# Performance work log

Measured on AMD Instinct MI355X. Metric: run time of the kernel, lower is better.

Reference implementation:

```python
import jax, jax.numpy as jnp
import numpy as np

B, N, E, H = 8, 512, 256, 8
HD = E // H
FF = 4 * E
TOPK = max(1, int(N * 0.2))
FW_MAX_DIST = 10      # default of get_shortest_path_matrix
EMB_MAX_IDX = 6       # spd encoder: max_dist(5) + 1
LN_EPS = 1e-5


def _layernorm(x, g, b):
    m = jnp.mean(x, axis=-1, keepdims=True)
    v = jnp.var(x, axis=-1, keepdims=True)
    return (x - m) / jnp.sqrt(v + LN_EPS) * g + b


def setup_inputs() -> dict:
    key = jax.random.key(0)
    ks = jax.random.split(key, 12)
    s = 0.02
    return {
        "x": jax.random.normal(ks[0], (B, N, E), jnp.float32),
        "adj": jax.random.uniform(ks[1], (B, N, N), jnp.float32),
        "emb_spd": (jax.random.normal(ks[2], (EMB_MAX_IDX + 1, H), jnp.float32) * s),
        "w_qkv": jax.random.normal(ks[3], (3 * E, E), jnp.float32) * s,
        "b_qkv": jnp.zeros((3 * E,), jnp.float32),
        "w_out": jax.random.normal(ks[4], (E, E), jnp.float32) * s,
        "b_out": jnp.zeros((E,), jnp.float32),
        "w_ff1": jax.random.normal(ks[5], (FF, E), jnp.float32) * s,
        "b_ff1": jnp.zeros((FF,), jnp.float32),
        "w_ff2": jax.random.normal(ks[6], (E, FF), jnp.float32) * s,
        "b_ff2": jnp.zeros((E,), jnp.float32),
        "g1": jnp.ones((E,), jnp.float32),
        "beta1": jnp.zeros((E,), jnp.float32),
        "g2": jnp.ones((E,), jnp.float32),
        "beta2": jnp.zeros((E,), jnp.float32),
        "w_pool": jax.random.normal(ks[7], (1, E), jnp.float32) * s,
        "b_pool": jnp.zeros((1,), jnp.float32),
    }


def _combined_mask(adj, emb_spd):
    # top-k per row -> binary adjacency via scatter
    _, idx = jax.lax.top_k(adj, TOPK)                       # [B,N,k]
    bi = jnp.arange(B)[:, None, None]
    ri = jnp.arange(N)[None, :, None]
    binary = jnp.zeros_like(adj).at[bi, ri, idx].set(1.0)   # [B,N,N]

    # Floyd-Warshall shortest paths
    dist = jnp.where(binary == 1.0, 1.0, jnp.inf)
    ids = jnp.arange(N)
    dist = dist.at[:, ids, ids].set(0.0)

    def body(k, d):
        return jnp.minimum(d, d[:, :, k][:, :, None] + d[:, k, :][:, None, :])

    dist = jax.lax.fori_loop(0, N, body, dist)
    dist_i = jnp.where(dist > FW_MAX_DIST, -1.0, dist).astype(jnp.int32)

    # spatial bias embedding: indices = clamp(dist+1, 0, max_dist+1)
    sp_idx = jnp.clip(dist_i + 1, 0, EMB_MAX_IDX)           # [B,N,N]
    bias = jnp.transpose(emb_spd[sp_idx], (0, 3, 1, 2))     # [B,H,N,N]

    base = jnp.where(binary == 0.0, -jnp.inf, 0.0)[:, None] # [B,1,N,N]
    return base + bias                                      # [B,H,N,N]


def reference(x, adj, emb_spd, w_qkv, b_qkv, w_out, b_out,
              w_ff1, b_ff1, w_ff2, b_ff2, g1, beta1, g2, beta2,
              w_pool, b_pool):
    mask = _combined_mask(adj, emb_spd)                     # [B,H,N,N]

    # multi-head self-attention (PyTorch MHA, post-norm encoder layer, eval)
    qkv = x @ w_qkv.T + b_qkv                               # [B,N,3E]
    q, k, v = jnp.split(qkv, 3, axis=-1)
    q = q.reshape(B, N, H, HD).transpose(0, 2, 1, 3)
    k = k.reshape(B, N, H, HD).transpose(0, 2, 1, 3)
    v = v.reshape(B, N, H, HD).transpose(0, 2, 1, 3)
    scores = jnp.einsum("bhqd,bhkd->bhqk", q, k) / np.sqrt(HD) + mask
    attn = jax.nn.softmax(scores, axis=-1)
    ctx = jnp.einsum("bhqk,bhkd->bhqd", attn, v)
    ctx = ctx.transpose(0, 2, 1, 3).reshape(B, N, E)
    attn_out = ctx @ w_out.T + b_out

    x1 = _layernorm(x + attn_out, g1, beta1)
    ff = jax.nn.relu(x1 @ w_ff1.T + b_ff1) @ w_ff2.T + b_ff2
    x2 = _layernorm(x1 + ff, g2, beta2)

    # attention pooling over nodes
    w = jax.nn.softmax(jnp.tanh(x2 @ w_pool.T + b_pool), axis=1)  # [B,N,1]
    return jnp.sum(x2 * w, axis=1)                          # [B,E]
```

## Files before the change

### kernel.cpp

```cpp
#include <hip/hip_runtime.h>
#include <math.h>


#define B_ 8
#define N_ 512
#define E_ 256
#define H_ 8
#define HD_ 32
#define TOPK_ 102

typedef __attribute__((ext_vector_type(8))) short bf16x8;
typedef __attribute__((ext_vector_type(4))) float f32x4;

__device__ __forceinline__ unsigned short f2b(float f) {
  unsigned u = __builtin_bit_cast(unsigned, f);
  return (unsigned short)((u + 0x7FFFu + ((u >> 16) & 1u)) >> 16);
}

__global__ __launch_bounds__(256) void cvt_topk(
    const float* __restrict__ adj, unsigned int* __restrict__ bits,
    const float* __restrict__ x, const float* __restrict__ wqkv,
    const float* __restrict__ wout, const float* __restrict__ wff1,
    const float* __restrict__ wff2, unsigned short* __restrict__ xb,
    unsigned short* __restrict__ wqkvb, unsigned short* __restrict__ woutb,
    unsigned short* __restrict__ wff1b, unsigned short* __restrict__ wff2b) {
  __shared__ unsigned int hist[1024];
  __shared__ float cval[64];
  __shared__ int cidx[64];
  __shared__ int s_cnt, s_bb, s_need;
  __shared__ unsigned int rowbits[16];
  __shared__ int wsum[4];
  const int t = threadIdx.x;

  if (blockIdx.x >= 4096) {
    int i = ((blockIdx.x - 4096) * 256 + t) * 4;
    const float* src;
    unsigned short* dst;
    int off;
    if (i < 1048576)      { src = x;    dst = xb;    off = i; }
    else if (i < 1245184) { src = wqkv; dst = wqkvb; off = i - 1048576; }
    else if (i < 1310720) { src = wout; dst = woutb; off = i - 1245184; }
    else if (i < 1572864) { src = wff1; dst = wff1b; off = i - 1310720; }
    else                  { src = wff2; dst = wff2b; off = i - 1572864; }
    float4 v = *(const float4*)(src + off);
    ushort4 o;
    o.x = f2b(v.x); o.y = f2b(v.y); o.z = f2b(v.z); o.w = f2b(v.w);
    *(ushort4*)(dst + off) = o;
    return;
  }
  const int row = blockIdx.x;
  const float* a = adj + (size_t)row * N_;
  const int lane = t & 63;
  const int wave = t >> 6;

  hist[t] = 0u; hist[t + 256] = 0u; hist[t + 512] = 0u; hist[t + 768] = 0u;
  if (t == 0) s_cnt = 0;
  float v0 = a[t];
  float v1 = a[t + 256];
  __syncthreads();
  const int b0 = min(1023, max(0, (int)(v0 * 1024.0f)));
  const int b1 = min(1023, max(0, (int)(v1 * 1024.0f)));
  atomicAdd(&hist[b0], 1u);
  atomicAdd(&hist[b1], 1u);
  __syncthreads();
  const int base = 1020 - 4 * t;
  const int h0 = (int)hist[base], h1 = (int)hist[base + 1];
  const int h2 = (int)hist[base + 2], h3 = (int)hist[base + 3];
  const int g = h0 + h1 + h2 + h3;
  int sc = g;
  #pragma unroll
  for (int off = 1; off < 64; off <<= 1) {
    int y = __shfl_up(sc, off);
    sc += (lane >= off) ? y : 0;
  }
  if (lane == 63) wsum[wave] = sc;
  __syncthreads();
  int wo = 0;
  for (int w = 0; w < wave; w++) wo += wsum[w];
  const int incl = sc + wo;
  const int excl = incl - g;
  if (excl < TOPK_ && incl >= TOPK_) {
    int cum = excl;
    int bb = base;
    const int hh[4] = {h3, h2, h1, h0};
    const int bs[4] = {base + 3, base + 2, base + 1, base};
    #pragma unroll
    for (int u = 0; u < 4; u++) {
      if (cum + hh[u] >= TOPK_) { bb = bs[u]; break; }
      cum += hh[u];
    }
    s_bb = bb;
    s_need = TOPK_ - cum;
  }
  __syncthreads();
  const int bb = s_bb;
  const int need = s_need;
  const bool sel0 = (b0 > bb);
  const bool sel1 = (b1 > bb);
  if (b0 == bb) { int p = atomicAdd(&s_cnt, 1); if (p < 64) { cval[p] = v0; cidx[p] = t; } }
  if (b1 == bb) { int p = atomicAdd(&s_cnt, 1); if (p < 64) { cval[p] = v1; cidx[p] = t + 256; } }
  unsigned long long m0 = __ballot(sel0);
  unsigned long long m1 = __ballot(sel1);
  if (lane == 0) {
    rowbits[2 * wave + 0] = (unsigned int)m0;
    rowbits[2 * wave + 1] = (unsigned int)(m0 >> 32);
    rowbits[8 + 2 * wave + 0] = (unsigned int)m1;
    rowbits[8 + 2 * wave + 1] = (unsigned int)(m1 >> 32);
  }
  __syncthreads();
  const int cnt = min(s_cnt, 64);
  for (int c = t; c < cnt; c += 256) {
    const float v = cval[c];
    const int idx = cidx[c];
    int r = 0;
    for (int j = 0; j < cnt; j++) {
      const float vj = cval[j];
      const int ij = cidx[j];
      if (vj > v || (vj == v && ij < idx)) r++;
    }
    if (r < need) atomicOr(&rowbits[idx >> 5], 1u << (idx & 31));
  }
  __syncthreads();
  if (t < 16) bits[(size_t)row * 16 + t] = rowbits[t];
}

__global__ __launch_bounds__(256) void gemm_mfma(
    const unsigned short* __restrict__ A, const unsigned short* __restrict__ W,
    const float* __restrict__ bias, const float* __restrict__ res,
    void* __restrict__ Cout, unsigned short* __restrict__ kG,
    unsigned short* __restrict__ vG, int M, int N, int K, int flags) {
  __shared__ __align__(16) unsigned short Af[8 * 64 * 8];
  __shared__ __align__(16) unsigned short Wf[8 * 64 * 8];
  const int tid = threadIdx.x;
  const int m0 = blockIdx.y * 64, n0 = blockIdx.x * 64;
  const int wave = tid >> 6, lane = tid & 63;
  const int wm = wave & 1, wn = wave >> 1;
  const int q = lane >> 4, l15 = lane & 15;
  const int r = tid >> 2, c0 = tid & 3;

  f32x4 acc[2][2];
  #pragma unroll
  for (int i = 0; i < 2; i++)
    #pragma unroll
    for (int j = 0; j < 2; j++) acc[i][j] = (f32x4){0.f, 0.f, 0.f, 0.f};

  const size_t arow = (size_t)(m0 + r) * K;
  const size_t wrow = (size_t)(n0 + r) * K;
  for (int k0 = 0; k0 < K; k0 += 64) {
    uint4 a0 = *(const uint4*)(A + arow + k0 + c0 * 8);
    uint4 a1 = *(const uint4*)(A + arow + k0 + (c0 + 4) * 8);
    uint4 w0 = *(const uint4*)(W + wrow + k0 + c0 * 8);
    uint4 w1 = *(const uint4*)(W + wrow + k0 + (c0 + 4) * 8);
    __syncthreads();
    {
      int kc = c0 >> 2, qq = c0 & 3;
      int s0 = ((r >> 4) * 2 + kc) * 64 + (r & 15) + qq * 16;
      int kc1 = (c0 + 4) >> 2, qq1 = (c0 + 4) & 3;
      int s1 = ((r >> 4) * 2 + kc1) * 64 + (r & 15) + qq1 * 16;
      *(uint4*)(Af + s0 * 8) = a0;
      *(uint4*)(Af + s1 * 8) = a1;
      *(uint4*)(Wf + s0 * 8) = w0;
      *(uint4*)(Wf + s1 * 8) = w1;
    }
    __syncthreads();
    #pragma unroll
    for (int kc = 0; kc < 2; kc++) {
      bf16x8 af[2], wf[2];
      #pragma unroll
      for (int mt = 0; mt < 2; mt++)
        af[mt] = *(const bf16x8*)(Af + (((wm * 2 + mt) * 2 + kc) * 64 + lane) * 8);
      #pragma unroll
      for (int nt = 0; nt < 2; nt++)
        wf[nt] = *(const bf16x8*)(Wf + (((wn * 2 + nt) * 2 + kc) * 64 + lane) * 8);
      #pragma unroll
      for (int mt = 0; mt < 2; mt++)
        #pragma unroll
        for (int nt = 0; nt < 2; nt++)
          acc[mt][nt] = __builtin_amdgcn_mfma_f32_16x16x32_bf16(af[mt], wf[nt], acc[mt][nt], 0, 0, 0);
    }
  }
  #pragma unroll
  for (int nt = 0; nt < 2; nt++) {
    const int col = n0 + (wn * 2 + nt) * 16 + l15;
    const float bv = bias[col];
    #pragma unroll
    for (int mt = 0; mt < 2; mt++) {
      const int rowb = m0 + (wm * 2 + mt) * 16 + q * 4;
      float ov[4];
      #pragma unroll
      for (int reg = 0; reg < 4; reg++) {
        float o = acc[mt][nt][reg] + bv;
        if (res) o += res[(size_t)(rowb + reg) * N + col];
        if (flags & 1) o = fmaxf(o, 0.f);
        ov[reg] = o;
      }
      if (flags & 4) {
        if (col < 256) {
          #pragma unroll
          for (int reg = 0; reg < 4; reg++)
            ((unsigned short*)Cout)[(size_t)(rowb + reg) * 256 + col] = f2b(ov[reg]);
        } else if (col < 512) {
          const int dfull = col - 256;
          const int hh2 = dfull >> 5, d = dfull & 31;
          const int q2 = d >> 3, sub = d & 7;
          const int bidx = rowb >> 9, j = rowb & 511;
          const int jt = j >> 6, jtile = (j >> 4) & 3, jl = j & 15;
          unsigned short* kp = kG +
              ((size_t)(((bidx * 8 + hh2) * 8 + jt) * 4 + jtile) * 64 + q2 * 16 + jl) * 8 + sub;
          kp[0] = f2b(ov[0]); kp[8] = f2b(ov[1]); kp[16] = f2b(ov[2]); kp[24] = f2b(ov[3]);
        } else {
          const int dfull = col - 512;
          const int hh2 = dfull >> 5, d = dfull & 31;
          const int dt = d >> 4, dl = d & 15;
          const int bidx = rowb >> 9, j = rowb & 511;
          const int jt = j >> 6, jj = j & 63;
          const int kc = jj >> 5, q2 = (jj >> 3) & 3, sub0 = jj & 7;
          ushort4 st;
          st.x = f2b(ov[0]); st.y = f2b(ov[1]); st.z = f2b(ov[2]); st.w = f2b(ov[3]);
          *(ushort4*)(vG +
              ((size_t)(((bidx * 8 + hh2) * 8 + jt) * 4 + dt * 2 + kc) * 64 + q2 * 16 + dl) * 8 + sub0) = st;
        }
      } else if (flags & 2) {
        #pragma unroll
        for (int reg = 0; reg < 4; reg++)
          ((unsigned short*)Cout)[(size_t)(rowb + reg) * N + col] = f2b(ov[reg]);
      } else {
        #pragma unroll
        for (int reg = 0; reg < 4; reg++)
          ((float*)Cout)[(size_t)(rowb + reg) * N + col] = ov[reg];
      }
    }
  }
}

__global__ __launch_bounds__(256) void attn_mfma(
    const unsigned short* __restrict__ qb, const unsigned short* __restrict__ kG,
    const unsigned short* __restrict__ vG, const unsigned int* __restrict__ bits,
    const float* __restrict__ emb, unsigned short* __restrict__ ctxo) {
  const int bx = blockIdx.x;
  const int ib = bx & 7;
  const int h = (bx >> 3) & 7;
  const int b = bx >> 6;
  const int tid = threadIdx.x;
  const int lane = tid & 63;
  const int wave = tid >> 6;
  const int q = lane >> 4, l15 = lane & 15;

  __shared__ __align__(16) unsigned int mrow[64 * 16];
  __shared__ __align__(16) unsigned short pF[4][2 * 64 * 8];

  {
    int rr = tid >> 2, wq = tid & 3;
    uint4 mw = *(const uint4*)(bits + ((size_t)(b * N_ + ib * 64 + rr)) * 16 + wq * 4);
    *(uint4*)(mrow + rr * 16 + wq * 4) = mw;
  }
  __syncthreads();

  const int i0w = ib * 64 + wave * 16;
  const bf16x8 qf = *(const bf16x8*)(qb + ((size_t)(b * N_ + i0w + l15)) * 256 + h * HD_ + q * 8);
  const float delta = emb[1 * H_ + h] - emb[2 * H_ + h];
  const float scale = 0.17677669529663687f;

  float m_run[4], l_run[4];
  #pragma unroll
  for (int e = 0; e < 4; e++) { m_run[e] = -1e30f; l_run[e] = 0.f; }
  f32x4 cacc[2];
  cacc[0] = (f32x4){0.f, 0.f, 0.f, 0.f};
  cacc[1] = (f32x4){0.f, 0.f, 0.f, 0.f};

  unsigned short* pbase = &pF[wave][0];
  const unsigned short* kb = kG + (size_t)(b * 8 + h) * 8 * 4 * 512;
  const unsigned short* vb = vG + (size_t)(b * 8 + h) * 8 * 4 * 512;

  #pragma unroll 1
  for (int jt = 0; jt < 8; jt++) {
    f32x4 s4[4];
    #pragma unroll
    for (int jtile = 0; jtile < 4; jtile++) {
      bf16x8 kf = *(const bf16x8*)(kb + (size_t)(jt * 4 + jtile) * 512 + lane * 8);
      s4[jtile] = __builtin_amdgcn_mfma_f32_16x16x32_bf16(qf, kf, (f32x4){0.f, 0.f, 0.f, 0.f}, 0, 0, 0);
    }
    unsigned long long mw64[4];
    #pragma unroll
    for (int reg = 0; reg < 4; reg++)
      mw64[reg] = *(const unsigned long long*)(mrow + (wave * 16 + q * 4 + reg) * 16 + jt * 2);
    float smat[4][4];
    #pragma unroll
    for (int jtile = 0; jtile < 4; jtile++) {
      #pragma unroll
      for (int reg = 0; reg < 4; reg++) {
        unsigned int w = (jtile & 2) ? (unsigned int)(mw64[reg] >> 32) : (unsigned int)mw64[reg];
        bool allowed = ((w >> ((jtile & 1) * 16 + l15)) & 1u) != 0u;
        int ig = ib * 64 + wave * 16 + q * 4 + reg;
        int jg = jt * 64 + jtile * 16 + l15;
        float s = s4[jtile][reg] * scale + ((jg == ig) ? delta : 0.f);
        smat[jtile][reg] = allowed ? s : -INFINITY;
      }
    }
    float alpha[4], pmat[4][4];
    #pragma unroll
    for (int reg = 0; reg < 4; reg++) {
      float mloc = fmaxf(fmaxf(smat[0][reg], smat[1][reg]), fmaxf(smat[2][reg], smat[3][reg]));
      #pragma unroll
      for (int off = 1; off < 16; off <<= 1) mloc = fmaxf(mloc, __shfl_xor(mloc, off));
      float mnew = fmaxf(m_run[reg], mloc);
      alpha[reg] = __expf(m_run[reg] - mnew);
      m_run[reg] = mnew;
      float ps = 0.f;
      #pragma unroll
      for (int jtile = 0; jtile < 4; jtile++) {
        float p = __expf(smat[jtile][reg] - mnew);
        pmat[jtile][reg] = p;
        ps += p;
      }
      #pragma unroll
      for (int off = 1; off < 16; off <<= 1) ps += __shfl_xor(ps, off);
      l_run[reg] = l_run[reg] * alpha[reg] + ps;
      cacc[0][reg] *= alpha[reg];
      cacc[1][reg] *= alpha[reg];
    }
    #pragma unroll
    for (int jtile = 0; jtile < 4; jtile++) {
      int j_l = jtile * 16 + l15;
      int sl = ((j_l >> 5) * 64 + ((j_l >> 3) & 3) * 16) * 8 + (j_l & 7);
      #pragma unroll
      for (int reg = 0; reg < 4; reg++)
        pbase[sl + (q * 4 + reg) * 8] = f2b(pmat[jtile][reg]);
    }
    #pragma unroll
    for (int kc = 0; kc < 2; kc++) {
      bf16x8 pf = *(const bf16x8*)(pbase + (kc * 64 + lane) * 8);
      #pragma unroll
      for (int dt = 0; dt < 2; dt++) {
        bf16x8 vf = *(const bf16x8*)(vb + (size_t)(jt * 4 + dt * 2 + kc) * 512 + lane * 8);
        cacc[dt] = __builtin_amdgcn_mfma_f32_16x16x32_bf16(pf, vf, cacc[dt], 0, 0, 0);
      }
    }
  }
  #pragma unroll
  for (int reg = 0; reg < 4; reg++) {
    const float linv = 1.f / l_run[reg];
    const size_t row = (size_t)(b * N_ + i0w + q * 4 + reg);
    #pragma unroll
    for (int dt = 0; dt < 2; dt++)
      ctxo[row * E_ + h * HD_ + dt * 16 + l15] = f2b(cacc[dt][reg] * linv);
  }
}

__global__ __launch_bounds__(256) void ln8_kernel(
    const float* __restrict__ t, const float* __restrict__ g,
    const float* __restrict__ be, float* __restrict__ out,
    unsigned short* __restrict__ outb) {
  __shared__ float sh[8];
  const int tid = threadIdx.x;
  const int wave = tid >> 6, lane = tid & 63;
  const float gv = g[tid], bev = be[tid];
  #pragma unroll 1
  for (int rr = 0; rr < 8; rr++) {
    const int row = blockIdx.x * 8 + rr;
    float v = t[(size_t)row * E_ + tid];
    float s = v, s2 = v * v;
    #pragma unroll
    for (int off = 32; off > 0; off >>= 1) {
      s += __shfl_xor(s, off);
      s2 += __shfl_xor(s2, off);
    }
    __syncthreads();
    if (lane == 0) { sh[wave] = s; sh[4 + wave] = s2; }
    __syncthreads();
    s = sh[0] + sh[1] + sh[2] + sh[3];
    s2 = sh[4] + sh[5] + sh[6] + sh[7];
    float mean = s * (1.f / 256.f);
    float var = s2 * (1.f / 256.f) - mean * mean;
    float inv = rsqrtf(var + 1e-5f);
    float o = (v - mean) * inv * gv + bev;
    out[(size_t)row * E_ + tid] = o;
    outb[(size_t)row * E_ + tid] = f2b(o);
  }
}

__global__ __launch_bounds__(256) void ln2pool_kernel(
    const float* __restrict__ t, const float* __restrict__ g,
    const float* __restrict__ be, const float* __restrict__ wp,
    const float* __restrict__ bp, float* __restrict__ partial,
    float* __restrict__ pwsum) {
  __shared__ float sh[8];
  const int tid = threadIdx.x;
  const int wave = tid >> 6, lane = tid & 63;
  const int c = blockIdx.x;
  const float gv = g[tid], bev = be[tid], wpv = wp[tid], bpv = bp[0];
  float pacc = 0.f, esum = 0.f;
  #pragma unroll 1
  for (int rr = 0; rr < 8; rr++) {
    const int row = c * 8 + rr;
    float v = t[(size_t)row * E_ + tid];
    float s = v, s2 = v * v;
    #pragma unroll
    for (int off = 32; off > 0; off >>= 1) {
      s += __shfl_xor(s, off);
      s2 += __shfl_xor(s2, off);
    }
    __syncthreads();
    if (lane == 0) { sh[wave] = s; sh[4 + wave] = s2; }
    __syncthreads();
    s = sh[0] + sh[1] + sh[2] + sh[3];
    s2 = sh[4] + sh[5] + sh[6] + sh[7];
    float mean = s * (1.f / 256.f);
    float var = s2 * (1.f / 256.f) - mean * mean;
    float inv = rsqrtf(var + 1e-5f);
    float o = (v - mean) * inv * gv + bev;
    float d = o * wpv;
    #pragma unroll
    for (int off = 32; off > 0; off >>= 1) d += __shfl_xor(d, off);
    __syncthreads();
    if (lane == 0) sh[wave] = d;
    __syncthreads();
    float dot = sh[0] + sh[1] + sh[2] + sh[3] + bpv;
    float e = __expf(tanhf(dot));
    pacc += e * o;
    esum += e;
  }
  partial[(size_t)c * E_ + tid] = pacc;
  if (tid == 0) pwsum[c] = esum;
}

__global__ __launch_bounds__(256) void pool_final(
    const float* __restrict__ partial, const float* __restrict__ pwsum,
    float* __restrict__ out) {
  const int b = blockIdx.x;
  const int tid = threadIdx.x;
  float acc = 0.f, ws = 0.f;
  #pragma unroll
  for (int c = 0; c < 64; c++) acc += partial[(size_t)(b * 64 + c) * E_ + tid];
  #pragma unroll
  for (int c = 0; c < 64; c++) ws += pwsum[b * 64 + c];
  out[b * E_ + tid] = acc / ws;
}

extern "C" void kernel_launch(void* const* d_in, const int* in_sizes, int n_in,
                              void* d_out, int out_size, void* d_ws, size_t ws_size,
                              hipStream_t stream) {
  (void)in_sizes; (void)n_in; (void)out_size; (void)ws_size;
  const float* x      = (const float*)d_in[0];
  const float* adj    = (const float*)d_in[1];
  const float* emb    = (const float*)d_in[2];
  const float* w_qkv  = (const float*)d_in[3];
  const float* b_qkv  = (const float*)d_in[4];
  const float* w_out  = (const float*)d_in[5];
  const float* b_out  = (const float*)d_in[6];
  const float* w_ff1  = (const float*)d_in[7];
  const float* b_ff1  = (const float*)d_in[8];
  const float* w_ff2  = (const float*)d_in[9];
  const float* b_ff2  = (const float*)d_in[10];
  const float* g1     = (const float*)d_in[11];
  const float* be1    = (const float*)d_in[12];
  const float* g2     = (const float*)d_in[13];
  const float* be2    = (const float*)d_in[14];
  const float* w_pool = (const float*)d_in[15];
  const float* b_pool = (const float*)d_in[16];

  char* ws = (char*)d_ws;
  unsigned int*   bits  = (unsigned int*)ws;
  unsigned short* xb    = (unsigned short*)(ws + 262144);
  unsigned short* qb    = (unsigned short*)(ws + 2359296);
  unsigned short* kG    = (unsigned short*)(ws + 4456448);
  unsigned short* vG    = (unsigned short*)(ws + 6553600);
  unsigned short* ctxb  = (unsigned short*)(ws + 8650752);
  float*          tbuf  = (float*)(ws + 10747904);
  float*          x1    = (float*)(ws + 14942208);
  unsigned short* x1b   = (unsigned short*)(ws + 19136512);
  unsigned short* hffb  = (unsigned short*)(ws + 21233664);
  unsigned short* wqkvb = (unsigned short*)(ws + 29622272);
  unsigned short* woutb = (unsigned short*)(ws + 30015488);
  unsigned short* wff1b = (unsigned short*)(ws + 30146560);
  unsigned short* wff2b = (unsigned short*)(ws + 30670848);
  float*          partial = (float*)(ws + 31195136);
  float*          pwsum   = (float*)(ws + 31719424);
  float*          outp  = (float*)d_out;

  const int M = B_ * N_;

  cvt_topk<<<4096 + 1792, 256, 0, stream>>>(adj, bits, x, w_qkv, w_out, w_ff1,
                                            w_ff2, xb, wqkvb, woutb, wff1b, wff2b);
  gemm_mfma<<<dim3(768 / 64, M / 64), 256, 0, stream>>>(
      xb, wqkvb, b_qkv, nullptr, qb, kG, vG, M, 768, E_, 4);
  attn_mfma<<<B_ * H_ * (N_ / 64), 256, 0, stream>>>(qb, kG, vG, bits, emb, ctxb);
  gemm_mfma<<<dim3(E_ / 64, M / 64), 256, 0, stream>>>(
      ctxb, woutb, b_out, x, tbuf, nullptr, nullptr, M, E_, E_, 0);
  ln8_kernel<<<M / 8, 256, 0, stream>>>(tbuf, g1, be1, x1, x1b);
  gemm_mfma<<<dim3(1024 / 64, M / 64), 256, 0, stream>>>(
      x1b, wff1b, b_ff1, nullptr, hffb, nullptr, nullptr, M, 1024, E_, 1 | 2);
  gemm_mfma<<<dim3(E_ / 64, M / 64), 256, 0, stream>>>(
      hffb, wff2b, b_ff2, x1, tbuf, nullptr, nullptr, M, E_, 1024, 0);
  ln2pool_kernel<<<M / 8, 256, 0, stream>>>(tbuf, g2, be2, w_pool, b_pool,
                                            partial, pwsum);
  pool_final<<<B_, 256, 0, stream>>>(partial, pwsum, outp);
}
```

Before: 178.5 us.

## Split-K the narrow GEMMs and fold bias/residual reduction into layernorm

The out-projection and FF2 GEMMs (N=256) now run with a split-K of 2 over blockIdx.z, each writing fp32 partials to separate buffers. The layernorm kernels then sum the two partials plus bias and residual. The GEMM K-step also doubles from 64 to 128 per LDS stage, halving the number of barrier pairs. This aims to raise occupancy for the narrow GEMMs (only 256 blocks before), at the cost of extra fp32 partial traffic and doubled shared memory.

```diff
diff --git a/kernel.cpp b/kernel.cpp
--- a/kernel.cpp
+++ b/kernel.cpp
@@ -128,11 +128,13 @@
     const unsigned short* __restrict__ A, const unsigned short* __restrict__ W,
     const float* __restrict__ bias, const float* __restrict__ res,
     void* __restrict__ Cout, unsigned short* __restrict__ kG,
-    unsigned short* __restrict__ vG, int M, int N, int K, int flags) {
-  __shared__ __align__(16) unsigned short Af[8 * 64 * 8];
-  __shared__ __align__(16) unsigned short Wf[8 * 64 * 8];
+    unsigned short* __restrict__ vG, int M, int N, int K, int ksplit, int flags) {
+  __shared__ __align__(16) unsigned short Af[16 * 64 * 8];
+  __shared__ __align__(16) unsigned short Wf[16 * 64 * 8];
   const int tid = threadIdx.x;
   const int m0 = blockIdx.y * 64, n0 = blockIdx.x * 64;
+  const int z = blockIdx.z;
+  const int Keff = K / ksplit;
   const int wave = tid >> 6, lane = tid & 63;
   const int wm = wave & 1, wn = wave >> 1;
   const int q = lane >> 4, l15 = lane & 15;
@@ -144,34 +146,32 @@
     #pragma unroll
     for (int j = 0; j < 2; j++) acc[i][j] = (f32x4){0.f, 0.f, 0.f, 0.f};
 
-  const size_t arow = (size_t)(m0 + r) * K;
-  const size_t wrow = (size_t)(n0 + r) * K;
-  for (int k0 = 0; k0 < K; k0 += 64) {
-    uint4 a0 = *(const uint4*)(A + arow + k0 + c0 * 8);
-    uint4 a1 = *(const uint4*)(A + arow + k0 + (c0 + 4) * 8);
-    uint4 w0 = *(const uint4*)(W + wrow + k0 + c0 * 8);
-    uint4 w1 = *(const uint4*)(W + wrow + k0 + (c0 + 4) * 8);
-    __syncthreads();
-    {
-      int kc = c0 >> 2, qq = c0 & 3;
-      int s0 = ((r >> 4) * 2 + kc) * 64 + (r & 15) + qq * 16;
-      int kc1 = (c0 + 4) >> 2, qq1 = (c0 + 4) & 3;
-      int s1 = ((r >> 4) * 2 + kc1) * 64 + (r & 15) + qq1 * 16;
-      *(uint4*)(Af + s0 * 8) = a0;
-      *(uint4*)(Af + s1 * 8) = a1;
-      *(uint4*)(Wf + s0 * 8) = w0;
-      *(uint4*)(Wf + s1 * 8) = w1;
-    }
-    __syncthreads();
-    #pragma unroll
-    for (int kc = 0; kc < 2; kc++) {
+  const size_t arow = (size_t)(m0 + r) * K + (size_t)z * Keff;
+  const size_t wrow = (size_t)(n0 + r) * K + (size_t)z * Keff;
+  for (int k0 = 0; k0 < Keff; k0 += 128) {
+    uint4 av[4], wv4[4];
+    #pragma unroll
+    for (int i = 0; i < 4; i++) {
+      av[i] = *(const uint4*)(A + arow + k0 + (c0 + 4 * i) * 8);
+      wv4[i] = *(const uint4*)(W + wrow + k0 + (c0 + 4 * i) * 8);
+    }
+    __syncthreads();
+    #pragma unroll
+    for (int i = 0; i < 4; i++) {
+      const int slot = ((r >> 4) * 4 + i) * 64 + c0 * 16 + (r & 15);
+      *(uint4*)(Af + slot * 8) = av[i];
+      *(uint4*)(Wf + slot * 8) = wv4[i];
+    }
+    __syncthreads();
+    #pragma unroll
+    for (int kc = 0; kc < 4; kc++) {
       bf16x8 af[2], wf[2];
       #pragma unroll
       for (int mt = 0; mt < 2; mt++)
-        af[mt] = *(const bf16x8*)(Af + (((wm * 2 + mt) * 2 + kc) * 64 + lane) * 8);
+        af[mt] = *(const bf16x8*)(Af + (((wm * 2 + mt) * 4 + kc) * 64 + lane) * 8);
       #pragma unroll
       for (int nt = 0; nt < 2; nt++)
-        wf[nt] = *(const bf16x8*)(Wf + (((wn * 2 + nt) * 2 + kc) * 64 + lane) * 8);
+        wf[nt] = *(const bf16x8*)(Wf + (((wn * 2 + nt) * 4 + kc) * 64 + lane) * 8);
       #pragma unroll
       for (int mt = 0; mt < 2; mt++)
         #pragma unroll
@@ -182,10 +182,17 @@
   #pragma unroll
   for (int nt = 0; nt < 2; nt++) {
     const int col = n0 + (wn * 2 + nt) * 16 + l15;
-    const float bv = bias[col];
+    const float bv = (flags & 8) ? 0.f : bias[col];
     #pragma unroll
     for (int mt = 0; mt < 2; mt++) {
       const int rowb = m0 + (wm * 2 + mt) * 16 + q * 4;
+      if (flags & 8) {
+        float* dst = (float*)Cout + (size_t)z * M * N;
+        #pragma unroll
+        for (int reg = 0; reg < 4; reg++)
+          dst[(size_t)(rowb + reg) * N + col] = acc[mt][nt][reg];
+        continue;
+      }
       float ov[4];
       #pragma unroll
       for (int reg = 0; reg < 4; reg++) {
@@ -348,17 +355,18 @@
 }
 
 __global__ __launch_bounds__(256) void ln8_kernel(
-    const float* __restrict__ t, const float* __restrict__ g,
-    const float* __restrict__ be, float* __restrict__ out,
-    unsigned short* __restrict__ outb) {
+    const float* __restrict__ t0, const float* __restrict__ t1,
+    const float* __restrict__ bias, const float* __restrict__ res,
+    const float* __restrict__ g, const float* __restrict__ be,
+    float* __restrict__ out, unsigned short* __restrict__ outb) {
   __shared__ float sh[8];
   const int tid = threadIdx.x;
   const int wave = tid >> 6, lane = tid & 63;
-  const float gv = g[tid], bev = be[tid];
+  const float gv = g[tid], bev = be[tid], bv = bias[tid];
   #pragma unroll 1
   for (int rr = 0; rr < 8; rr++) {
-    const int row = blockIdx.x * 8 + rr;
-    float v = t[(size_t)row * E_ + tid];
+    const size_t idx = (size_t)(blockIdx.x * 8 + rr) * E_ + tid;
+    float v = t0[idx] + t1[idx] + bv + res[idx];
     float s = v, s2 = v * v;
     #pragma unroll
     for (int off = 32; off > 0; off >>= 1) {
@@ -374,26 +382,28 @@
     float var = s2 * (1.f / 256.f) - mean * mean;
     float inv = rsqrtf(var + 1e-5f);
     float o = (v - mean) * inv * gv + bev;
-    out[(size_t)row * E_ + tid] = o;
-    outb[(size_t)row * E_ + tid] = f2b(o);
+    out[idx] = o;
+    outb[idx] = f2b(o);
   }
 }
 
 __global__ __launch_bounds__(256) void ln2pool_kernel(
-    const float* __restrict__ t, const float* __restrict__ g,
-    const float* __restrict__ be, const float* __restrict__ wp,
-    const float* __restrict__ bp, float* __restrict__ partial,
-    float* __restrict__ pwsum) {
+    const float* __restrict__ t0, const float* __restrict__ t1,
+    const float* __restrict__ bias, const float* __restrict__ res,
+    const float* __restrict__ g, const float* __restrict__ be,
+    const float* __restrict__ wp, const float* __restrict__ bp,
+    float* __restrict__ partial, float* __restrict__ pwsum) {
   __shared__ float sh[8];
   const int tid = threadIdx.x;
   const int wave = tid >> 6, lane = tid & 63;
   const int c = blockIdx.x;
-  const float gv = g[tid], bev = be[tid], wpv = wp[tid], bpv = bp[0];
+  const float gv = g[tid], bev = be[tid], bv = bias[tid];
+  const float wpv = wp[tid], bpv = bp[0];
   float pacc = 0.f, esum = 0.f;
   #pragma unroll 1
   for (int rr = 0; rr < 8; rr++) {
-    const int row = c * 8 + rr;
-    float v = t[(size_t)row * E_ + tid];
+    const size_t idx = (size_t)(c * 8 + rr) * E_ + tid;
+    float v = t0[idx] + t1[idx] + bv + res[idx];
     float s = v, s2 = v * v;
     #pragma unroll
     for (int off = 32; off > 0; off >>= 1) {
@@ -466,33 +476,35 @@
   unsigned short* kG    = (unsigned short*)(ws + 4456448);
   unsigned short* vG    = (unsigned short*)(ws + 6553600);
   unsigned short* ctxb  = (unsigned short*)(ws + 8650752);
-  float*          tbuf  = (float*)(ws + 10747904);
-  float*          x1    = (float*)(ws + 14942208);
-  unsigned short* x1b   = (unsigned short*)(ws + 19136512);
-  unsigned short* hffb  = (unsigned short*)(ws + 21233664);
-  unsigned short* wqkvb = (unsigned short*)(ws + 29622272);
-  unsigned short* woutb = (unsigned short*)(ws + 30015488);
-  unsigned short* wff1b = (unsigned short*)(ws + 30146560);
-  unsigned short* wff2b = (unsigned short*)(ws + 30670848);
-  float*          partial = (float*)(ws + 31195136);
-  float*          pwsum   = (float*)(ws + 31719424);
+  float*          tp0   = (float*)(ws + 10747904);
+  float*          tp1   = (float*)(ws + 14942208);
+  float*          x1    = (float*)(ws + 19136512);
+  unsigned short* x1b   = (unsigned short*)(ws + 23330816);
+  unsigned short* hffb  = (unsigned short*)(ws + 25427968);
+  unsigned short* wqkvb = (unsigned short*)(ws + 33816576);
+  unsigned short* woutb = (unsigned short*)(ws + 34209792);
+  unsigned short* wff1b = (unsigned short*)(ws + 34340864);
+  unsigned short* wff2b = (unsigned short*)(ws + 34865152);
+  float*          partial = (float*)(ws + 35389440);
+  float*          pwsum   = (float*)(ws + 35913728);
   float*          outp  = (float*)d_out;
+  (void)tp1;
 
   const int M = B_ * N_;
 
   cvt_topk<<<4096 + 1792, 256, 0, stream>>>(adj, bits, x, w_qkv, w_out, w_ff1,
                                             w_ff2, xb, wqkvb, woutb, wff1b, wff2b);
-  gemm_mfma<<<dim3(768 / 64, M / 64), 256, 0, stream>>>(
-      xb, wqkvb, b_qkv, nullptr, qb, kG, vG, M, 768, E_, 4);
+  gemm_mfma<<<dim3(768 / 64, M / 64, 1), 256, 0, stream>>>(
+      xb, wqkvb, b_qkv, nullptr, qb, kG, vG, M, 768, E_, 1, 4);
   attn_mfma<<<B_ * H_ * (N_ / 64), 256, 0, stream>>>(qb, kG, vG, bits, emb, ctxb);
-  gemm_mfma<<<dim3(E_ / 64, M / 64), 256, 0, stream>>>(
-      ctxb, woutb, b_out, x, tbuf, nullptr, nullptr, M, E_, E_, 0);
-  ln8_kernel<<<M / 8, 256, 0, stream>>>(tbuf, g1, be1, x1, x1b);
-  gemm_mfma<<<dim3(1024 / 64, M / 64), 256, 0, stream>>>(
-      x1b, wff1b, b_ff1, nullptr, hffb, nullptr, nullptr, M, 1024, E_, 1 | 2);
-  gemm_mfma<<<dim3(E_ / 64, M / 64), 256, 0, stream>>>(
-      hffb, wff2b, b_ff2, x1, tbuf, nullptr, nullptr, M, E_, 1024, 0);
-  ln2pool_kernel<<<M / 8, 256, 0, stream>>>(tbuf, g2, be2, w_pool, b_pool,
-                                            partial, pwsum);
+  gemm_mfma<<<dim3(E_ / 64, M / 64, 2), 256, 0, stream>>>(
+      ctxb, woutb, nullptr, nullptr, tp0, nullptr, nullptr, M, E_, E_, 2, 8);
+  ln8_kernel<<<M / 8, 256, 0, stream>>>(tp0, tp1, b_out, x, g1, be1, x1, x1b);
+  gemm_mfma<<<dim3(1024 / 64, M / 64, 1), 256, 0, stream>>>(
+      x1b, wff1b, b_ff1, nullptr, hffb, nullptr, nullptr, M, 1024, E_, 1, 1 | 2);
+  gemm_mfma<<<dim3(E_ / 64, M / 64, 2), 256, 0, stream>>>(
+      hffb, wff2b, nullptr, nullptr, tp0, nullptr, nullptr, M, E_, 1024, 2, 8);
+  ln2pool_kernel<<<M / 8, 256, 0, stream>>>(tp0, tp1, b_ff2, x1, g2, be2,
+                                            w_pool, b_pool, partial, pwsum);
   pool_final<<<B_, 256, 0, stream>>>(partial, pwsum, outp);
 }
```

New measurement: 228.8 us. 1.28x slower.

## Fuse fp32-to-bf16 conversion into GEMM loads and add 32-row GEMM tile

Applied to the files above, without the earlier changes.

Removes the separate conversion pass that wrote bf16 copies of x and all weights. The GEMMs now read fp32 directly and round to bf16 while staging tiles into shared memory, which saves a full write-plus-read of the converted tensors. The N=256 GEMMs (out-proj, FF2) switch to a 32x64 tile kernel, doubling the block count so the GPU is better filled. In exchange, weights get reconverted by every block that loads them, and the fp32 reads move twice the bytes.

```diff
diff --git a/kernel.cpp b/kernel.cpp
--- a/kernel.cpp
+++ b/kernel.cpp
@@ -17,13 +17,19 @@
   return (unsigned short)((u + 0x7FFFu + ((u >> 16) & 1u)) >> 16);
 }
 
-__global__ __launch_bounds__(256) void cvt_topk(
-    const float* __restrict__ adj, unsigned int* __restrict__ bits,
-    const float* __restrict__ x, const float* __restrict__ wqkv,
-    const float* __restrict__ wout, const float* __restrict__ wff1,
-    const float* __restrict__ wff2, unsigned short* __restrict__ xb,
-    unsigned short* __restrict__ wqkvb, unsigned short* __restrict__ woutb,
-    unsigned short* __restrict__ wff1b, unsigned short* __restrict__ wff2b) {
+__device__ __forceinline__ uint4 cvt8(const float* __restrict__ p) {
+  float4 a = *(const float4*)p;
+  float4 b = *(const float4*)(p + 4);
+  uint4 o;
+  o.x = (unsigned)f2b(a.x) | ((unsigned)f2b(a.y) << 16);
+  o.y = (unsigned)f2b(a.z) | ((unsigned)f2b(a.w) << 16);
+  o.z = (unsigned)f2b(b.x) | ((unsigned)f2b(b.y) << 16);
+  o.w = (unsigned)f2b(b.z) | ((unsigned)f2b(b.w) << 16);
+  return o;
+}
+
+__global__ __launch_bounds__(256) void topk_kernel(const float* __restrict__ adj,
+                                                   unsigned int* __restrict__ bits) {
   __shared__ unsigned int hist[1024];
   __shared__ float cval[64];
   __shared__ int cidx[64];
@@ -31,23 +37,6 @@
   __shared__ unsigned int rowbits[16];
   __shared__ int wsum[4];
   const int t = threadIdx.x;
-
-  if (blockIdx.x >= 4096) {
-    int i = ((blockIdx.x - 4096) * 256 + t) * 4;
-    const float* src;
-    unsigned short* dst;
-    int off;
-    if (i < 1048576)      { src = x;    dst = xb;    off = i; }
-    else if (i < 1245184) { src = wqkv; dst = wqkvb; off = i - 1048576; }
-    else if (i < 1310720) { src = wout; dst = woutb; off = i - 1245184; }
-    else if (i < 1572864) { src = wff1; dst = wff1b; off = i - 1310720; }
-    else                  { src = wff2; dst = wff2b; off = i - 1572864; }
-    float4 v = *(const float4*)(src + off);
-    ushort4 o;
-    o.x = f2b(v.x); o.y = f2b(v.y); o.z = f2b(v.z); o.w = f2b(v.w);
-    *(ushort4*)(dst + off) = o;
-    return;
-  }
   const int row = blockIdx.x;
   const float* a = adj + (size_t)row * N_;
   const int lane = t & 63;
@@ -124,8 +113,8 @@
   if (t < 16) bits[(size_t)row * 16 + t] = rowbits[t];
 }
 
-__global__ __launch_bounds__(256) void gemm_mfma(
-    const unsigned short* __restrict__ A, const unsigned short* __restrict__ W,
+__global__ __launch_bounds__(256) void gemm64(
+    const void* __restrict__ A, const void* __restrict__ W,
     const float* __restrict__ bias, const float* __restrict__ res,
     void* __restrict__ Cout, unsigned short* __restrict__ kG,
     unsigned short* __restrict__ vG, int M, int N, int K, int flags) {
@@ -147,10 +136,21 @@
   const size_t arow = (size_t)(m0 + r) * K;
   const size_t wrow = (size_t)(n0 + r) * K;
   for (int k0 = 0; k0 < K; k0 += 64) {
-    uint4 a0 = *(const uint4*)(A + arow + k0 + c0 * 8);
-    uint4 a1 = *(const uint4*)(A + arow + k0 + (c0 + 4) * 8);
-    uint4 w0 = *(const uint4*)(W + wrow + k0 + c0 * 8);
-    uint4 w1 = *(const uint4*)(W + wrow + k0 + (c0 + 4) * 8);
+    uint4 a0, a1, w0, w1;
+    if (flags & 16) {
+      a0 = cvt8((const float*)A + arow + k0 + c0 * 8);
+      a1 = cvt8((const float*)A + arow + k0 + (c0 + 4) * 8);
+    } else {
+      a0 = *(const uint4*)((const unsigned short*)A + arow + k0 + c0 * 8);
+      a1 = *(const uint4*)((const unsigned short*)A + arow + k0 + (c0 + 4) * 8);
+    }
+    if (flags & 32) {
+      w0 = cvt8((const float*)W + wrow + k0 + c0 * 8);
+      w1 = cvt8((const float*)W + wrow + k0 + (c0 + 4) * 8);
+    } else {
+      w0 = *(const uint4*)((const unsigned short*)W + wrow + k0 + c0 * 8);
+      w1 = *(const uint4*)((const unsigned short*)W + wrow + k0 + (c0 + 4) * 8);
+    }
     __syncthreads();
     {
       int kc = c0 >> 2, qq = c0 & 3;
@@ -233,6 +233,63 @@
   }
 }
 
+__global__ __launch_bounds__(256) void gemm32(
+    const unsigned short* __restrict__ A, const float* __restrict__ W,
+    const float* __restrict__ bias, const float* __restrict__ res,
+    float* __restrict__ Cout, int M, int N, int K) {
+  __shared__ __align__(16) unsigned short Af[4 * 64 * 8];
+  __shared__ __align__(16) unsigned short Wf[8 * 64 * 8];
+  const int tid = threadIdx.x;
+  const int m0 = blockIdx.y * 32, n0 = blockIdx.x * 64;
+  const int wave = tid >> 6, lane = tid & 63;
+  const int wm = wave & 1, wn = wave >> 1;
+  const int q = lane >> 4, l15 = lane & 15;
+  const int ar = tid >> 3, ac = tid & 7;
+  const int wr = tid >> 2, wc = tid & 3;
+
+  f32x4 acc[2];
+  acc[0] = (f32x4){0.f, 0.f, 0.f, 0.f};
+  acc[1] = (f32x4){0.f, 0.f, 0.f, 0.f};
+
+  const size_t arow = (size_t)(m0 + ar) * K;
+  const size_t wrow = (size_t)(n0 + wr) * K;
+  for (int k0 = 0; k0 < K; k0 += 64) {
+    uint4 av = *(const uint4*)(A + arow + k0 + ac * 8);
+    uint4 w0 = cvt8(W + wrow + k0 + wc * 8);
+    uint4 w1 = cvt8(W + wrow + k0 + (wc + 4) * 8);
+    __syncthreads();
+    {
+      const int kca = ac >> 2, qqa = ac & 3;
+      *(uint4*)(Af + (((ar >> 4) * 2 + kca) * 64 + qqa * 16 + (ar & 15)) * 8) = av;
+      const int s0 = ((wr >> 4) * 2 + 0) * 64 + wc * 16 + (wr & 15);
+      const int s1 = ((wr >> 4) * 2 + 1) * 64 + wc * 16 + (wr & 15);
+      *(uint4*)(Wf + s0 * 8) = w0;
+      *(uint4*)(Wf + s1 * 8) = w1;
+    }
+    __syncthreads();
+    #pragma unroll
+    for (int kc = 0; kc < 2; kc++) {
+      bf16x8 af = *(const bf16x8*)(Af + ((wm * 2 + kc) * 64 + lane) * 8);
+      #pragma unroll
+      for (int nt = 0; nt < 2; nt++) {
+        bf16x8 wf = *(const bf16x8*)(Wf + (((wn * 2 + nt) * 2 + kc) * 64 + lane) * 8);
+        acc[nt] = __builtin_amdgcn_mfma_f32_16x16x32_bf16(af, wf, acc[nt], 0, 0, 0);
+      }
+    }
+  }
+  #pragma unroll
+  for (int nt = 0; nt < 2; nt++) {
+    const int col = n0 + (wn * 2 + nt) * 16 + l15;
+    const float bv = bias[col];
+    const int rowb = m0 + wm * 16 + q * 4;
+    #pragma unroll
+    for (int reg = 0; reg < 4; reg++) {
+      float o = acc[nt][reg] + bv + res[(size_t)(rowb + reg) * N + col];
+      Cout[(size_t)(rowb + reg) * N + col] = o;
+    }
+  }
+}
+
 __global__ __launch_bounds__(256) void attn_mfma(
     const unsigned short* __restrict__ qb, const unsigned short* __restrict__ kG,
     const unsigned short* __restrict__ vG, const unsigned int* __restrict__ bits,
@@ -461,37 +518,31 @@
 
   char* ws = (char*)d_ws;
   unsigned int*   bits  = (unsigned int*)ws;
-  unsigned short* xb    = (unsigned short*)(ws + 262144);
-  unsigned short* qb    = (unsigned short*)(ws + 2359296);
-  unsigned short* kG    = (unsigned short*)(ws + 4456448);
-  unsigned short* vG    = (unsigned short*)(ws + 6553600);
-  unsigned short* ctxb  = (unsigned short*)(ws + 8650752);
-  float*          tbuf  = (float*)(ws + 10747904);
-  float*          x1    = (float*)(ws + 14942208);
-  unsigned short* x1b   = (unsigned short*)(ws + 19136512);
-  unsigned short* hffb  = (unsigned short*)(ws + 21233664);
-  unsigned short* wqkvb = (unsigned short*)(ws + 29622272);
-  unsigned short* woutb = (unsigned short*)(ws + 30015488);
-  unsigned short* wff1b = (unsigned short*)(ws + 30146560);
-  unsigned short* wff2b = (unsigned short*)(ws + 30670848);
-  float*          partial = (float*)(ws + 31195136);
-  float*          pwsum   = (float*)(ws + 31719424);
+  unsigned short* qb    = (unsigned short*)(ws + 262144);
+  unsigned short* kG    = (unsigned short*)(ws + 2359296);
+  unsigned short* vG    = (unsigned short*)(ws + 4456448);
+  unsigned short* ctxb  = (unsigned short*)(ws + 6553600);
+  float*          tbuf  = (float*)(ws + 8650752);
+  float*          x1    = (float*)(ws + 12845056);
+  unsigned short* x1b   = (unsigned short*)(ws + 17039360);
+  unsigned short* hffb  = (unsigned short*)(ws + 19136512);
+  float*          partial = (float*)(ws + 27525120);
+  float*          pwsum   = (float*)(ws + 28049408);
   float*          outp  = (float*)d_out;
 
   const int M = B_ * N_;
 
-  cvt_topk<<<4096 + 1792, 256, 0, stream>>>(adj, bits, x, w_qkv, w_out, w_ff1,
-                                            w_ff2, xb, wqkvb, woutb, wff1b, wff2b);
-  gemm_mfma<<<dim3(768 / 64, M / 64), 256, 0, stream>>>(
-      xb, wqkvb, b_qkv, nullptr, qb, kG, vG, M, 768, E_, 4);
+  topk_kernel<<<M, 256, 0, stream>>>(adj, bits);
+  gemm64<<<dim3(768 / 64, M / 64), 256, 0, stream>>>(
+      x, w_qkv, b_qkv, nullptr, qb, kG, vG, M, 768, E_, 4 | 16 | 32);
   attn_mfma<<<B_ * H_ * (N_ / 64), 256, 0, stream>>>(qb, kG, vG, bits, emb, ctxb);
-  gemm_mfma<<<dim3(E_ / 64, M / 64), 256, 0, stream>>>(
-      ctxb, woutb, b_out, x, tbuf, nullptr, nullptr, M, E_, E_, 0);
+  gemm32<<<dim3(E_ / 64, M / 32), 256, 0, stream>>>(
+      ctxb, w_out, b_out, x, tbuf, M, E_, E_);
   ln8_kernel<<<M / 8, 256, 0, stream>>>(tbuf, g1, be1, x1, x1b);
-  gemm_mfma<<<dim3(1024 / 64, M / 64), 256, 0, stream>>>(
-      x1b, wff1b, b_ff1, nullptr, hffb, nullptr, nullptr, M, 1024, E_, 1 | 2);
-  gemm_mfma<<<dim3(E_ / 64, M / 64), 256, 0, stream>>>(
-      hffb, wff2b, b_ff2, x1, tbuf, nullptr, nullptr, M, E_, 1024, 0);
+  gemm64<<<dim3(1024 / 64, M / 64), 256, 0, stream>>>(
+      x1b, w_ff1, b_ff1, nullptr, hffb, nullptr, nullptr, M, 1024, E_, 1 | 2 | 32);
+  gemm32<<<dim3(E_ / 64, M / 32), 256, 0, stream>>>(
+      hffb, w_ff2, b_ff2, x1, tbuf, M, E_, 1024);
   ln2pool_kernel<<<M / 8, 256, 0, stream>>>(tbuf, g2, be2, w_pool, b_pool,
                                             partial, pwsum);
   pool_final<<<B_, 256, 0, stream>>>(partial, pwsum, outp);
```

Result: slower. 182.2 us (+2.1%).
